# Kernel tuning notes

Measured on AMD Instinct MI355X. Metric: run time of the kernel, lower is better.

## Reference

```python
import jax, jax.numpy as jnp
import numpy as np

B, C, H, W = 4, 256, 48, 48
KD, NH, AR = 32, 8, 4
D = AR * KD            # 128, value dim per head
NHKD = NH * KD         # 256
DH = NH * D            # 1024
EPS = 1e-5


def _bn(y, g, b):
    # BN with fresh running stats (mean=0, var=1): y*g/sqrt(1+eps)+b, over channel dim
    s = g / jnp.sqrt(jnp.float32(1.0) + EPS)
    return y * s[None, :, None] + b[None, :, None]


def setup_inputs() -> dict:
    key = jax.random.key(0)
    ks = jax.random.split(key, 13)
    w = lambda k, sh: jax.random.normal(k, sh, jnp.float32) * 0.05
    g = lambda k, sh: 1.0 + jax.random.normal(k, sh, jnp.float32) * 0.05
    return {
        "x": jax.random.normal(ks[0], (B, C, H, W), jnp.float32),
        "wq": w(ks[1], (NHKD, C)), "gq": g(ks[2], (NHKD,)), "bq": w(ks[3], (NHKD,)),
        "wk": w(ks[4], (NHKD, C)), "gk": g(ks[5], (NHKD,)), "bk": w(ks[6], (NHKD,)),
        "wv": w(ks[7], (DH, C)),   "gv": g(ks[8], (DH,)),   "bv": w(ks[9], (DH,)),
        "wp": w(ks[10], (C, DH)),  "gp": g(ks[11], (C,)),   "bp": w(ks[12], (C,)),
    }


def reference(x, wq, gq, bq, wk, gk, bk, wv, gv, bv, wp, gp, bp):
    b, c, h, w = x.shape
    n = h * w
    xf = x.reshape(b, c, n)                                   # [B,C,N]
    # 1x1 conv == channel matmul, then BN
    q = _bn(jnp.einsum('oc,bcn->bon', wq, xf), gq, bq).reshape(b, NH, KD, n)
    k = _bn(jnp.einsum('oc,bcn->bon', wk, xf), gk, bk).reshape(b, NH, KD, n)
    v = _bn(jnp.einsum('oc,bcn->bon', wv, xf), gv, bv).reshape(b, NH, D, n)
    # NOTE: original forward does NOT apply self.scale
    attn = jax.nn.softmax(jnp.einsum('bhkn,bhkm->bhnm', q, k), axis=-1)  # [B,H,N,N]
    xx = jnp.einsum('bhnm,bhdm->bhdn', attn, v).reshape(b, DH, n)        # [B,DH,N]
    out = _bn(jnp.einsum('oc,bcn->bon', wp, jax.nn.relu(xx)), gp, bp)
    return out.reshape(b, c, h, w)
```

## Files before the change

kernel.cpp:

```cpp
#include <hip/hip_runtime.h>

#define BB 4
#define C 256
#define HW 2304
#define NH 8
#define KD 32
#define D 128
#define DH 1024
#define MQ 256

typedef unsigned short bf16u;
typedef __attribute__((ext_vector_type(8))) short short8;
typedef __attribute__((ext_vector_type(4))) short bfx4;
typedef __attribute__((ext_vector_type(4))) float f32x4;

__device__ __forceinline__ float b2f(bf16u u) {
    return __uint_as_float(((unsigned)u) << 16);
}
__device__ __forceinline__ bf16u f2b(float f) {
    unsigned u = __float_as_uint(f);
    return (bf16u)((u + 0x7fffu + ((u >> 16) & 1u)) >> 16);
}
__device__ __forceinline__ unsigned pk2(float a, float b) {
    return ((unsigned)f2b(b) << 16) | (unsigned)f2b(a);
}

#if __has_builtin(__builtin_amdgcn_mfma_f32_16x16x16bf16_1k)
__device__ __forceinline__ f32x4 mfma16(bfx4 a, bfx4 b, f32x4 c) {
    return __builtin_amdgcn_mfma_f32_16x16x16bf16_1k(a, b, c, 0, 0, 0);
}
#else
__device__ __forceinline__ f32x4 mfma16(bfx4 a, bfx4 b, f32x4 c) {
    asm volatile("v_mfma_f32_16x16x16_bf16 %0, %1, %2, %0"
                 : "+v"(c) : "v"(a), "v"(b));
    return c;
}
#endif

__device__ __forceinline__ void glds16(const bf16u* g, bf16u* l) {
    __builtin_amdgcn_global_load_lds(
        (const __attribute__((address_space(1))) unsigned int*)g,
        (__attribute__((address_space(3))) unsigned int*)l,
        16, 0, 0);
}

__global__ __launch_bounds__(256) void xtrans(const float* __restrict__ x,
                                              bf16u* __restrict__ xT)
{
    const int c0 = blockIdx.x * 64, n0 = blockIdx.y * 64, b = blockIdx.z;
    const int t = threadIdx.x;
    __shared__ float tile[64][68];

    const float* xb = x + (size_t)b * C * HW;
    #pragma unroll
    for (int rr = 0; rr < 4; ++rr) {
        const int cl = rr*16 + (t >> 4);
        float4 v = *(const float4*)(xb + (size_t)(c0 + cl) * HW + n0 + (t & 15)*4);
        tile[cl][(t&15)*4+0] = v.x; tile[cl][(t&15)*4+1] = v.y;
        tile[cl][(t&15)*4+2] = v.z; tile[cl][(t&15)*4+3] = v.w;
    }
    __syncthreads();
    const int nl = t >> 2, ch = t & 3;
    short8 v0, v1;
    #pragma unroll
    for (int kk = 0; kk < 8; ++kk) v0[kk] = (short)f2b(tile[ch*16+kk][nl]);
    #pragma unroll
    for (int kk = 0; kk < 8; ++kk) v1[kk] = (short)f2b(tile[ch*16+8+kk][nl]);
    bf16u* dst = xT + ((size_t)b*HW + n0 + nl) * C + c0 + ch*16;
    *(short8*)(dst)     = v0;
    *(short8*)(dst + 8) = v1;
}

__global__ __launch_bounds__(256, 2) void qkv_gemm(
    const float* __restrict__ wq, const float* __restrict__ wk, const float* __restrict__ wv,
    const float* __restrict__ gq, const float* __restrict__ bq,
    const float* __restrict__ gk, const float* __restrict__ bk,
    const float* __restrict__ gv, const float* __restrict__ bv,
    const bf16u* __restrict__ xT,
    bf16u* __restrict__ qT, bf16u* __restrict__ kT, bf16u* __restrict__ vO)
{
    const int mt = blockIdx.x, ntb = blockIdx.y, b = blockIdx.z;
    const int r0 = mt * 128, c0 = ntb * 128;
    const int t = threadIdx.x, w = t >> 6, l = t & 63;
    const int l15 = l & 15, q = l >> 4;
    const int wr = w >> 1, wc = w & 1;

    const float* wsel; int rloc;
    if (r0 < 256)      { wsel = wq; rloc = r0; }
    else if (r0 < 512) { wsel = wk; rloc = r0 - 256; }
    else               { wsel = wv; rloc = r0 - 512; }

    __shared__ bf16u smem[16384];

    const bf16u* xb = xT + (size_t)b * HW * C;

    const int sA0 = (w*2+0)*64 + l, sA1 = (w*2+1)*64 + l;
    const float* gA0 = wsel + (size_t)(rloc + (sA0>>2)) * C + (sA0&3)*8;
    const float* gA1 = wsel + (size_t)(rloc + (sA1>>2)) * C + (sA1&3)*8;
    const bf16u* gB0 = xb + (size_t)(c0 + (sA0>>2)) * C + (sA0&3)*8;
    const bf16u* gB1 = xb + (size_t)(c0 + (sA1>>2)) * C + (sA1&3)*8;

    f32x4 acc[4][4];
    #pragma unroll
    for (int i = 0; i < 4; ++i)
        #pragma unroll
        for (int j = 0; j < 4; ++j) { acc[i][j][0]=0.f; acc[i][j][1]=0.f; acc[i][j][2]=0.f; acc[i][j][3]=0.f; }

    auto stageB = [&](int k0, int bb) {
        bf16u* Bs = smem + 8192 + bb*4096;
        glds16(gB0 + k0, Bs + (w*2+0)*512);
        glds16(gB1 + k0, Bs + (w*2+1)*512);
    };
    auto stageA = [&](int k0, int bb) {
        bf16u* As = smem + bb*4096;
        #pragma unroll
        for (int jj = 0; jj < 2; ++jj) {
            const float* ga = jj ? gA1 : gA0;
            const int    s  = jj ? sA1 : sA0;
            float4 a = *(const float4*)(ga + k0);
            float4 c = *(const float4*)(ga + k0 + 4);
            short8 v;
            v[0]=(short)f2b(a.x); v[1]=(short)f2b(a.y); v[2]=(short)f2b(a.z); v[3]=(short)f2b(a.w);
            v[4]=(short)f2b(c.x); v[5]=(short)f2b(c.y); v[6]=(short)f2b(c.z); v[7]=(short)f2b(c.w);
            *(short8*)(As + s*8) = v;
        }
    };

    stageB(0, 0); stageA(0, 0);
    for (int it = 0; it < 8; ++it) {
        __syncthreads();
        if (it < 7) { stageB((it+1)*32, (it+1)&1); stageA((it+1)*32, (it+1)&1); }
        const bf16u* A = smem + (it&1)*4096;
        const bf16u* B = smem + 8192 + (it&1)*4096;
        short8 af[4], bf[4];
        #pragma unroll
        for (int i = 0; i < 4; ++i) af[i] = *(const short8*)(A + (wr*64 + i*16 + l15)*32 + q*8);
        #pragma unroll
        for (int j = 0; j < 4; ++j) bf[j] = *(const short8*)(B + (wc*64 + j*16 + l15)*32 + q*8);
        #pragma unroll
        for (int i = 0; i < 4; ++i)
            #pragma unroll
            for (int j = 0; j < 4; ++j)
                acc[i][j] = __builtin_amdgcn_mfma_f32_16x16x32_bf16(af[i], bf[j], acc[i][j], 0, 0, 0);
    }

    const float rs = rsqrtf(1.0f + 1e-5f);
    int ncol[4];
    #pragma unroll
    for (int j = 0; j < 4; ++j) ncol[j] = c0 + wc*64 + j*16 + l15;

    if (r0 < 512) {
        const float* g   = (r0 < 256) ? gq : gk;
        const float* bb_ = (r0 < 256) ? bq : bk;
        bf16u* dst = (r0 < 256) ? qT : kT;
        const int ocb = (r0 & 255) + wr*64;
        #pragma unroll
        for (int i = 0; i < 4; ++i)
            #pragma unroll
            for (int r = 0; r < 4; ++r) {
                const int oc = ocb + i*16 + q*4 + r;
                const float s = g[oc]*rs, bi = bb_[oc];
                const size_t base = ((size_t)(b*NH + (oc>>5)) * HW) * KD + (oc & 31);
                #pragma unroll
                for (int j = 0; j < 4; ++j)
                    dst[base + (size_t)ncol[j]*KD] = f2b(acc[i][j][r]*s + bi);
            }
    } else {
        const int db = (r0 - 512) + wr*64;
        bf16u* dst = vO + (size_t)b * DH * HW;
        #pragma unroll
        for (int i = 0; i < 4; ++i)
            #pragma unroll
            for (int r = 0; r < 4; ++r) {
                const int d = db + i*16 + q*4 + r;
                const float s = gv[d]*rs, bi = bv[d];
                #pragma unroll
                for (int j = 0; j < 4; ++j)
                    dst[(size_t)d*HW + ncol[j]] = f2b(acc[i][j][r]*s + bi);
            }
    }
}

__global__ __launch_bounds__(256, 3) void attn_mfma(
    const bf16u* __restrict__ qT, const bf16u* __restrict__ kT,
    const bf16u* __restrict__ vg, bf16u* __restrict__ xg)
{
    const int nt = blockIdx.x, h = blockIdx.y, b = blockIdx.z;
    const int n0 = nt * 128;
    const int t = threadIdx.x;
    const int w = t >> 6, l = t & 63, l15 = l & 15, q = l >> 4;

    const bf16u* qTh = qT + (size_t)(b*NH + h) * HW * KD;
    const bf16u* kTh = kT + (size_t)(b*NH + h) * HW * KD;
    const bf16u* vh  = vg + ((size_t)b*DH + (size_t)h*D) * HW;

    __shared__ bf16u smem[20480];

    short8 qf0 = *(const short8*)(qTh + (size_t)(n0 + w*32 +      l15) * KD + q*8);
    short8 qf1 = *(const short8*)(qTh + (size_t)(n0 + w*32 + 16 + l15) * KD + q*8);

    f32x4 o[2][8];
    #pragma unroll
    for (int a = 0; a < 2; ++a)
        #pragma unroll
        for (int d = 0; d < 8; ++d) { o[a][d][0]=0.f; o[a][d][1]=0.f; o[a][d][2]=0.f; o[a][d][3]=0.f; }
    float psum0 = 0.f, psum1 = 0.f;
    const f32x4 zero = {0.f, 0.f, 0.f, 0.f};

    auto stage = [&](int m0, int bb) {
        bf16u* Ks = smem + bb*2048;
        bf16u* Vs = smem + 4096 + bb*8192;
        glds16(kTh + (size_t)m0*KD + (w*64 + l)*8, Ks + w*512);
        #pragma unroll
        for (int j = 0; j < 4; ++j) {
            const int s = (w*4 + j)*64 + l;
            const int d = s >> 3, c = s & 7, cg = c ^ (d & 7);
            glds16(vh + (size_t)d*HW + m0 + cg*8, Vs + (w*4 + j)*512);
        }
    };

    stage(0, 0);
    for (int mt = 0; mt < 36; ++mt) {
        __syncthreads();
        if (mt < 35) stage((mt+1)*64, (mt+1)&1);
        const bf16u* Ks = smem + (mt&1)*2048;
        const bf16u* Vs = smem + 4096 + (mt&1)*8192;

        f32x4 st0[4], st1[4];
        #pragma unroll
        for (int kt = 0; kt < 4; ++kt) {
            short8 kf = *(const short8*)(Ks + (kt*16 + l15)*KD + q*8);
            st0[kt] = __builtin_amdgcn_mfma_f32_16x16x32_bf16(kf, qf0, zero, 0, 0, 0);
            st1[kt] = __builtin_amdgcn_mfma_f32_16x16x32_bf16(kf, qf1, zero, 0, 0, 0);
        }

        bfx4 pk0[4], pk1[4];
        #pragma unroll
        for (int kt = 0; kt < 4; ++kt) {
            float p0 = __expf(st0[kt][0]), p1 = __expf(st0[kt][1]);
            float p2 = __expf(st0[kt][2]), p3 = __expf(st0[kt][3]);
            psum0 += (p0 + p1) + (p2 + p3);
            uint2 uu; uu.x = pk2(p0, p1); uu.y = pk2(p2, p3);
            pk0[kt] = __builtin_bit_cast(bfx4, uu);
            float r0_ = __expf(st1[kt][0]), r1 = __expf(st1[kt][1]);
            float r2 = __expf(st1[kt][2]), r3 = __expf(st1[kt][3]);
            psum1 += (r0_ + r1) + (r2 + r3);
            uint2 vv; vv.x = pk2(r0_, r1); vv.y = pk2(r2, r3);
            pk1[kt] = __builtin_bit_cast(bfx4, vv);
        }

        #pragma unroll
        for (int kt = 0; kt < 4; ++kt) {
            #pragma unroll
            for (int dt = 0; dt < 8; ++dt) {
                const int d = dt*16 + l15;
                const int cm = kt*2 + (q >> 1);
                bfx4 vf = *(const bfx4*)(Vs + d*64 + ((cm ^ (d & 7)) * 8) + (q & 1)*4);
                o[0][dt] = mfma16(pk0[kt], vf, o[0][dt]);
                o[1][dt] = mfma16(pk1[kt], vf, o[1][dt]);
            }
        }
    }

    psum0 += __shfl_xor(psum0, 16); psum0 += __shfl_xor(psum0, 32);
    psum1 += __shfl_xor(psum1, 16); psum1 += __shfl_xor(psum1, 32);
    float inv0[4], inv1[4];
    #pragma unroll
    for (int r = 0; r < 4; ++r) {
        inv0[r] = 1.0f / __shfl(psum0, q*4 + r);
        inv1[r] = 1.0f / __shfl(psum1, q*4 + r);
    }
    __syncthreads();
    bf16u* Od = smem + w * 4352;
    #pragma unroll
    for (int dt = 0; dt < 8; ++dt)
        #pragma unroll
        for (int r = 0; r < 4; ++r) {
            float v0 = fmaxf(o[0][dt][r] * inv0[r], 0.f);
            float v1 = fmaxf(o[1][dt][r] * inv1[r], 0.f);
            Od[(     q*4 + r)*136 + dt*16 + l15] = f2b(v0);
            Od[(16 + q*4 + r)*136 + dt*16 + l15] = f2b(v1);
        }
    bf16u* xb = xg + ((size_t)b*HW + n0 + w*32) * DH + h*D;
    #pragma unroll
    for (int rr = 0; rr < 2; ++rr) {
        const int row = rr*16 + (l >> 2), c = l & 3;
        #pragma unroll
        for (int kk = 0; kk < 4; ++kk)
            *(short8*)(xb + (size_t)row*DH + c*32 + kk*8) =
                *(const short8*)(Od + row*136 + c*32 + kk*8);
    }
}

__global__ __launch_bounds__(256, 4) void out_gemm(
    const float* __restrict__ wp, const float* __restrict__ gp, const float* __restrict__ bp,
    const bf16u* __restrict__ xx, float* __restrict__ out)
{
    const int mt = blockIdx.x, ntb = blockIdx.y, b = blockIdx.z;
    const int r0 = mt * 64, c0 = ntb * 64;
    const int t = threadIdx.x, w = t >> 6, l = t & 63;
    const int l15 = l & 15, q = l >> 4;
    const int wr = w >> 1, wc = w & 1;

    __shared__ bf16u smem[8192];

    const bf16u* xb = xx + (size_t)b * HW * DH;

    const float* gA = wp + (size_t)(r0 + (t>>2)) * DH + (t&3)*8;
    const bf16u* gB = xb + (size_t)(c0 + (t>>2)) * DH + (t&3)*8;

    f32x4 acc[2][2];
    #pragma unroll
    for (int i = 0; i < 2; ++i)
        #pragma unroll
        for (int j = 0; j < 2; ++j) { acc[i][j][0]=0.f; acc[i][j][1]=0.f; acc[i][j][2]=0.f; acc[i][j][3]=0.f; }

    auto stage = [&](int k0, int bb) {
        glds16(gB + k0, smem + 4096 + bb*2048 + w*512);
        float4 a = *(const float4*)(gA + k0);
        float4 c = *(const float4*)(gA + k0 + 4);
        short8 v;
        v[0]=(short)f2b(a.x); v[1]=(short)f2b(a.y); v[2]=(short)f2b(a.z); v[3]=(short)f2b(a.w);
        v[4]=(short)f2b(c.x); v[5]=(short)f2b(c.y); v[6]=(short)f2b(c.z); v[7]=(short)f2b(c.w);
        *(short8*)(smem + bb*2048 + t*8) = v;
    };

    stage(0, 0);
    for (int it = 0; it < 32; ++it) {
        __syncthreads();
        if (it < 31) stage((it+1)*32, (it+1)&1);
        const bf16u* A = smem + (it&1)*2048;
        const bf16u* B = smem + 4096 + (it&1)*2048;
        short8 af[2], bf[2];
        #pragma unroll
        for (int i = 0; i < 2; ++i) af[i] = *(const short8*)(A + (wr*32 + i*16 + l15)*32 + q*8);
        #pragma unroll
        for (int j = 0; j < 2; ++j) bf[j] = *(const short8*)(B + (wc*32 + j*16 + l15)*32 + q*8);
        #pragma unroll
        for (int i = 0; i < 2; ++i)
            #pragma unroll
            for (int j = 0; j < 2; ++j)
                acc[i][j] = __builtin_amdgcn_mfma_f32_16x16x32_bf16(af[i], bf[j], acc[i][j], 0, 0, 0);
    }

    const float rs = rsqrtf(1.0f + 1e-5f);
    #pragma unroll
    for (int i = 0; i < 2; ++i)
        #pragma unroll
        for (int r = 0; r < 4; ++r) {
            const int oc = r0 + wr*32 + i*16 + q*4 + r;
            const float s = gp[oc]*rs, bi = bp[oc];
            #pragma unroll
            for (int j = 0; j < 2; ++j) {
                const int n = c0 + wc*32 + j*16 + l15;
                out[((size_t)b*C + oc)*HW + n] = acc[i][j][r]*s + bi;
            }
        }
}

extern "C" void kernel_launch(void* const* d_in, const int* in_sizes, int n_in,
                              void* d_out, int out_size, void* d_ws, size_t ws_size,
                              hipStream_t stream) {
    const float* x  = (const float*)d_in[0];
    const float* wq = (const float*)d_in[1];
    const float* gq = (const float*)d_in[2];
    const float* bq = (const float*)d_in[3];
    const float* wk = (const float*)d_in[4];
    const float* gk = (const float*)d_in[5];
    const float* bk = (const float*)d_in[6];
    const float* wv = (const float*)d_in[7];
    const float* gv = (const float*)d_in[8];
    const float* bv = (const float*)d_in[9];
    const float* wp = (const float*)d_in[10];
    const float* gp = (const float*)d_in[11];
    const float* bp = (const float*)d_in[12];
    float* out = (float*)d_out;

    bf16u* qw = (bf16u*)d_ws;
    bf16u* kw = qw + (size_t)BB * MQ * HW;
    bf16u* vw = kw + (size_t)BB * MQ * HW;
    bf16u* xw = vw + (size_t)BB * DH * HW;
    bf16u* xTb = xw;

    hipLaunchKernelGGL(xtrans, dim3(4, 36, BB), dim3(256), 0, stream, x, xTb);
    hipLaunchKernelGGL(qkv_gemm, dim3(12, 18, BB), dim3(256), 0, stream,
                       wq, wk, wv, gq, bq, gk, bk, gv, bv, xTb, qw, kw, vw);
    hipLaunchKernelGGL(attn_mfma, dim3(18, NH, BB), dim3(256), 0, stream,
                       qw, kw, vw, xw);
    hipLaunchKernelGGL(out_gemm, dim3(4, 36, BB), dim3(256), 0, stream,
                       wp, gp, bp, xw, out);
}
```

Measured before the change: 239.4 us.

## Pre-fold BN into bf16 weights, triple-buffer GEMMs, coalesce QKV stores, use exp2

A new prep kernel converts the Q/K/V weights to bf16 once per call. It folds the BN scale into them, plus a log2(e) factor for Q, and writes a combined bias vector. This lets qkv_gemm stage both operands with direct global-to-LDS loads in a three-stage pipeline. The QKV epilogue now goes through LDS with a swizzled layout so Q/K/V are written as 16-byte coalesced stores instead of scattered 2-byte writes. Attention switches to exp2 and 16x16x32 MFMAs for the PV product, and out_gemm uses 64-wide K tiles with triple buffering; this costs an extra launch and more LDS per block.

```diff
diff --git a/kernel.cpp b/kernel.cpp
--- a/kernel.cpp
+++ b/kernel.cpp
@@ -13,35 +13,64 @@
 typedef __attribute__((ext_vector_type(8))) short short8;
 typedef __attribute__((ext_vector_type(4))) short bfx4;
 typedef __attribute__((ext_vector_type(4))) float f32x4;
-
-__device__ __forceinline__ float b2f(bf16u u) {
-    return __uint_as_float(((unsigned)u) << 16);
-}
+typedef __attribute__((ext_vector_type(4))) unsigned ux4;
+typedef __attribute__((ext_vector_type(2))) unsigned ux2;
+
+union U8 { ux4 u; short8 s; };
+union V8 { short8 s; bfx4 h[2]; };
+
 __device__ __forceinline__ bf16u f2b(float f) {
     unsigned u = __float_as_uint(f);
     return (bf16u)((u + 0x7fffu + ((u >> 16) & 1u)) >> 16);
 }
-__device__ __forceinline__ unsigned pk2(float a, float b) {
-    return ((unsigned)f2b(b) << 16) | (unsigned)f2b(a);
-}
-
-#if __has_builtin(__builtin_amdgcn_mfma_f32_16x16x16bf16_1k)
-__device__ __forceinline__ f32x4 mfma16(bfx4 a, bfx4 b, f32x4 c) {
-    return __builtin_amdgcn_mfma_f32_16x16x16bf16_1k(a, b, c, 0, 0, 0);
-}
-#else
-__device__ __forceinline__ f32x4 mfma16(bfx4 a, bfx4 b, f32x4 c) {
-    asm volatile("v_mfma_f32_16x16x16_bf16 %0, %1, %2, %0"
-                 : "+v"(c) : "v"(a), "v"(b));
-    return c;
-}
-#endif
+__device__ __forceinline__ unsigned pkb(float a, float b) {
+    return __builtin_amdgcn_perm(__float_as_uint(b) + 0x8000u,
+                                 __float_as_uint(a) + 0x8000u, 0x07060302u);
+}
 
 __device__ __forceinline__ void glds16(const bf16u* g, bf16u* l) {
     __builtin_amdgcn_global_load_lds(
         (const __attribute__((address_space(1))) unsigned int*)g,
         (__attribute__((address_space(3))) unsigned int*)l,
         16, 0, 0);
+}
+
+#define MFMA32 __builtin_amdgcn_mfma_f32_16x16x32_bf16
+
+__global__ __launch_bounds__(256) void prep(
+    const float* __restrict__ wq, const float* __restrict__ wk, const float* __restrict__ wv,
+    const float* __restrict__ gq, const float* __restrict__ bq,
+    const float* __restrict__ gk, const float* __restrict__ bk,
+    const float* __restrict__ gv, const float* __restrict__ bv,
+    bf16u* __restrict__ Wc, float* __restrict__ biasc)
+{
+    const float rs = rsqrtf(1.0f + 1e-5f);
+    const float L2E = 1.4426950408889634f;
+    const int t = threadIdx.x, blk = blockIdx.x;
+    if (blk < 192) {
+        const int idx = (blk*256 + t) * 8;
+        const int row = idx >> 8;
+        const float* src; float sc;
+        if (idx < 65536)       { src = wq + idx;            sc = gq[row]*rs*L2E; }
+        else if (idx < 131072) { src = wk + (idx - 65536);  sc = gk[row-256]*rs; }
+        else                   { src = wv + (idx - 131072); sc = gv[row-512]*rs; }
+        float4 a = *(const float4*)(src);
+        float4 c = *(const float4*)(src + 4);
+        ux4 v;
+        v.x = pkb(a.x*sc, a.y*sc); v.y = pkb(a.z*sc, a.w*sc);
+        v.z = pkb(c.x*sc, c.y*sc); v.w = pkb(c.z*sc, c.w*sc);
+        *(ux4*)(Wc + idx) = v;
+    } else {
+        #pragma unroll
+        for (int k = 0; k < 6; ++k) {
+            const int r = k*256 + t;
+            float v;
+            if (r < 256)      v = bq[r] * L2E;
+            else if (r < 512) v = bk[r - 256];
+            else              v = bv[r - 512];
+            biasc[r] = v;
+        }
+    }
 }
 
 __global__ __launch_bounds__(256) void xtrans(const float* __restrict__ x,
@@ -71,11 +100,8 @@
     *(short8*)(dst + 8) = v1;
 }
 
-__global__ __launch_bounds__(256, 2) void qkv_gemm(
-    const float* __restrict__ wq, const float* __restrict__ wk, const float* __restrict__ wv,
-    const float* __restrict__ gq, const float* __restrict__ bq,
-    const float* __restrict__ gk, const float* __restrict__ bk,
-    const float* __restrict__ gv, const float* __restrict__ bv,
+__global__ __launch_bounds__(256, 3) void qkv_gemm(
+    const bf16u* __restrict__ Wc, const float* __restrict__ biasc,
     const bf16u* __restrict__ xT,
     bf16u* __restrict__ qT, bf16u* __restrict__ kT, bf16u* __restrict__ vO)
 {
@@ -85,18 +111,13 @@
     const int l15 = l & 15, q = l >> 4;
     const int wr = w >> 1, wc = w & 1;
 
-    const float* wsel; int rloc;
-    if (r0 < 256)      { wsel = wq; rloc = r0; }
-    else if (r0 < 512) { wsel = wk; rloc = r0 - 256; }
-    else               { wsel = wv; rloc = r0 - 512; }
-
-    __shared__ bf16u smem[16384];
+    __shared__ bf16u smem[24576];
 
     const bf16u* xb = xT + (size_t)b * HW * C;
 
     const int sA0 = (w*2+0)*64 + l, sA1 = (w*2+1)*64 + l;
-    const float* gA0 = wsel + (size_t)(rloc + (sA0>>2)) * C + (sA0&3)*8;
-    const float* gA1 = wsel + (size_t)(rloc + (sA1>>2)) * C + (sA1&3)*8;
+    const bf16u* gA0 = Wc + (size_t)(r0 + (sA0>>2)) * C + (sA0&3)*8;
+    const bf16u* gA1 = Wc + (size_t)(r0 + (sA1>>2)) * C + (sA1&3)*8;
     const bf16u* gB0 = xb + (size_t)(c0 + (sA0>>2)) * C + (sA0&3)*8;
     const bf16u* gB1 = xb + (size_t)(c0 + (sA1>>2)) * C + (sA1&3)*8;
 
@@ -106,78 +127,101 @@
         #pragma unroll
         for (int j = 0; j < 4; ++j) { acc[i][j][0]=0.f; acc[i][j][1]=0.f; acc[i][j][2]=0.f; acc[i][j][3]=0.f; }
 
-    auto stageB = [&](int k0, int bb) {
-        bf16u* Bs = smem + 8192 + bb*4096;
+    auto stage = [&](int it2, int bb) {
+        const int k0 = it2 * 32;
+        bf16u* As = smem + bb*4096;
+        bf16u* Bs = smem + 12288 + bb*4096;
+        glds16(gA0 + k0, As + (w*2+0)*512);
+        glds16(gA1 + k0, As + (w*2+1)*512);
         glds16(gB0 + k0, Bs + (w*2+0)*512);
         glds16(gB1 + k0, Bs + (w*2+1)*512);
     };
-    auto stageA = [&](int k0, int bb) {
-        bf16u* As = smem + bb*4096;
-        #pragma unroll
-        for (int jj = 0; jj < 2; ++jj) {
-            const float* ga = jj ? gA1 : gA0;
-            const int    s  = jj ? sA1 : sA0;
-            float4 a = *(const float4*)(ga + k0);
-            float4 c = *(const float4*)(ga + k0 + 4);
-            short8 v;
-            v[0]=(short)f2b(a.x); v[1]=(short)f2b(a.y); v[2]=(short)f2b(a.z); v[3]=(short)f2b(a.w);
-            v[4]=(short)f2b(c.x); v[5]=(short)f2b(c.y); v[6]=(short)f2b(c.z); v[7]=(short)f2b(c.w);
-            *(short8*)(As + s*8) = v;
-        }
-    };
-
-    stageB(0, 0); stageA(0, 0);
+
+    const bool isV = (r0 >= 512);
+    stage(0, 0); stage(1, 1);
     for (int it = 0; it < 8; ++it) {
         __syncthreads();
-        if (it < 7) { stageB((it+1)*32, (it+1)&1); stageA((it+1)*32, (it+1)&1); }
-        const bf16u* A = smem + (it&1)*4096;
-        const bf16u* B = smem + 8192 + (it&1)*4096;
+        if (it + 2 < 8) stage(it + 2, (it + 2) % 3);
+        const bf16u* A = smem + (it % 3) * 4096;
+        const bf16u* B = smem + 12288 + (it % 3) * 4096;
         short8 af[4], bf[4];
         #pragma unroll
         for (int i = 0; i < 4; ++i) af[i] = *(const short8*)(A + (wr*64 + i*16 + l15)*32 + q*8);
         #pragma unroll
         for (int j = 0; j < 4; ++j) bf[j] = *(const short8*)(B + (wc*64 + j*16 + l15)*32 + q*8);
-        #pragma unroll
-        for (int i = 0; i < 4; ++i)
-            #pragma unroll
-            for (int j = 0; j < 4; ++j)
-                acc[i][j] = __builtin_amdgcn_mfma_f32_16x16x32_bf16(af[i], bf[j], acc[i][j], 0, 0, 0);
-    }
-
-    const float rs = rsqrtf(1.0f + 1e-5f);
-    int ncol[4];
-    #pragma unroll
-    for (int j = 0; j < 4; ++j) ncol[j] = c0 + wc*64 + j*16 + l15;
-
-    if (r0 < 512) {
-        const float* g   = (r0 < 256) ? gq : gk;
-        const float* bb_ = (r0 < 256) ? bq : bk;
-        bf16u* dst = (r0 < 256) ? qT : kT;
-        const int ocb = (r0 & 255) + wr*64;
-        #pragma unroll
-        for (int i = 0; i < 4; ++i)
-            #pragma unroll
-            for (int r = 0; r < 4; ++r) {
-                const int oc = ocb + i*16 + q*4 + r;
-                const float s = g[oc]*rs, bi = bb_[oc];
-                const size_t base = ((size_t)(b*NH + (oc>>5)) * HW) * KD + (oc & 31);
+        if (!isV) {
+            #pragma unroll
+            for (int i = 0; i < 4; ++i)
                 #pragma unroll
                 for (int j = 0; j < 4; ++j)
-                    dst[base + (size_t)ncol[j]*KD] = f2b(acc[i][j][r]*s + bi);
-            }
-    } else {
-        const int db = (r0 - 512) + wr*64;
-        bf16u* dst = vO + (size_t)b * DH * HW;
-        #pragma unroll
-        for (int i = 0; i < 4; ++i)
-            #pragma unroll
-            for (int r = 0; r < 4; ++r) {
-                const int d = db + i*16 + q*4 + r;
-                const float s = gv[d]*rs, bi = bv[d];
+                    acc[i][j] = MFMA32(af[i], bf[j], acc[i][j], 0, 0, 0);
+        } else {
+            #pragma unroll
+            for (int i = 0; i < 4; ++i)
                 #pragma unroll
                 for (int j = 0; j < 4; ++j)
-                    dst[(size_t)d*HW + ncol[j]] = f2b(acc[i][j][r]*s + bi);
+                    acc[i][j] = MFMA32(bf[j], af[i], acc[i][j], 0, 0, 0);
+        }
+    }
+
+    __syncthreads();
+    bf16u* Od = smem + w * 4096;
+
+    if (!isV) {
+        float bC[4][4];
+        #pragma unroll
+        for (int i = 0; i < 4; ++i)
+            #pragma unroll
+            for (int r = 0; r < 4; ++r)
+                bC[i][r] = biasc[r0 + wr*64 + i*16 + q*4 + r];
+        #pragma unroll
+        for (int i = 0; i < 4; ++i)
+            #pragma unroll
+            for (int j = 0; j < 4; ++j) {
+                float y0 = acc[i][j][0] + bC[i][0];
+                float y1 = acc[i][j][1] + bC[i][1];
+                float y2 = acc[i][j][2] + bC[i][2];
+                float y3 = acc[i][j][3] + bC[i][3];
+                ux2 pk; pk.x = pkb(y0, y1); pk.y = pkb(y2, y3);
+                const int row = j*16 + l15;
+                const int ch  = (i*2 + (q >> 1)) ^ (l15 & 7);
+                *(ux2*)(Od + row*64 + ch*8 + (q & 1)*4) = pk;
             }
+        bf16u* dst = (r0 < 256) ? qT : kT;
+        const int n = c0 + wc*64 + l;
+        #pragma unroll
+        for (int c = 0; c < 8; ++c) {
+            short8 v = *(const short8*)(Od + l*64 + ((c ^ (l & 7)) * 8));
+            const int ocg = (r0 & 255) + wr*64 + c*8;
+            const int h = ocg >> 5, kd0 = ocg & 31;
+            *(short8*)(dst + ((size_t)(b*NH + h) * HW + n) * KD + kd0) = v;
+        }
+    } else {
+        float bC[4];
+        #pragma unroll
+        for (int i = 0; i < 4; ++i)
+            bC[i] = biasc[r0 + wr*64 + i*16 + l15];
+        #pragma unroll
+        for (int i = 0; i < 4; ++i)
+            #pragma unroll
+            for (int j = 0; j < 4; ++j) {
+                float y0 = acc[i][j][0] + bC[i];
+                float y1 = acc[i][j][1] + bC[i];
+                float y2 = acc[i][j][2] + bC[i];
+                float y3 = acc[i][j][3] + bC[i];
+                ux2 pk; pk.x = pkb(y0, y1); pk.y = pkb(y2, y3);
+                const int row = i*16 + l15;
+                const int ch  = (j*2 + (q >> 1)) ^ (l15 & 7);
+                *(ux2*)(Od + row*64 + ch*8 + (q & 1)*4) = pk;
+            }
+        bf16u* dst = vO + (size_t)b * DH * HW;
+        const int d = (r0 - 512) + wr*64 + l;
+        #pragma unroll
+        for (int c = 0; c < 8; ++c) {
+            short8 v = *(const short8*)(Od + l*64 + ((c ^ (l & 7)) * 8));
+            const int n = c0 + wc*64 + c*8;
+            *(short8*)(dst + (size_t)d * HW + n) = v;
+        }
     }
 }
 
@@ -230,34 +274,45 @@
         #pragma unroll
         for (int kt = 0; kt < 4; ++kt) {
             short8 kf = *(const short8*)(Ks + (kt*16 + l15)*KD + q*8);
-            st0[kt] = __builtin_amdgcn_mfma_f32_16x16x32_bf16(kf, qf0, zero, 0, 0, 0);
-            st1[kt] = __builtin_amdgcn_mfma_f32_16x16x32_bf16(kf, qf1, zero, 0, 0, 0);
-        }
-
-        bfx4 pk0[4], pk1[4];
+            st0[kt] = MFMA32(kf, qf0, zero, 0, 0, 0);
+            st1[kt] = MFMA32(kf, qf1, zero, 0, 0, 0);
+        }
+
+        unsigned dA0[4], dB0[4], dA1[4], dB1[4];
         #pragma unroll
         for (int kt = 0; kt < 4; ++kt) {
-            float p0 = __expf(st0[kt][0]), p1 = __expf(st0[kt][1]);
-            float p2 = __expf(st0[kt][2]), p3 = __expf(st0[kt][3]);
+            float p0 = __builtin_amdgcn_exp2f(st0[kt][0]);
+            float p1 = __builtin_amdgcn_exp2f(st0[kt][1]);
+            float p2 = __builtin_amdgcn_exp2f(st0[kt][2]);
+            float p3 = __builtin_amdgcn_exp2f(st0[kt][3]);
             psum0 += (p0 + p1) + (p2 + p3);
-            uint2 uu; uu.x = pk2(p0, p1); uu.y = pk2(p2, p3);
-            pk0[kt] = __builtin_bit_cast(bfx4, uu);
-            float r0_ = __expf(st1[kt][0]), r1 = __expf(st1[kt][1]);
-            float r2 = __expf(st1[kt][2]), r3 = __expf(st1[kt][3]);
-            psum1 += (r0_ + r1) + (r2 + r3);
-            uint2 vv; vv.x = pk2(r0_, r1); vv.y = pk2(r2, r3);
-            pk1[kt] = __builtin_bit_cast(bfx4, vv);
-        }
-
-        #pragma unroll
-        for (int kt = 0; kt < 4; ++kt) {
+            dA0[kt] = pkb(p0, p1); dB0[kt] = pkb(p2, p3);
+            float r0_ = __builtin_amdgcn_exp2f(st1[kt][0]);
+            float r1_ = __builtin_amdgcn_exp2f(st1[kt][1]);
+            float r2_ = __builtin_amdgcn_exp2f(st1[kt][2]);
+            float r3_ = __builtin_amdgcn_exp2f(st1[kt][3]);
+            psum1 += (r0_ + r1_) + (r2_ + r3_);
+            dA1[kt] = pkb(r0_, r1_); dB1[kt] = pkb(r2_, r3_);
+        }
+
+        #pragma unroll
+        for (int kh = 0; kh < 2; ++kh) {
+            U8 u0, u1;
+            u0.u[0] = dA0[kh*2];   u0.u[1] = dB0[kh*2];
+            u0.u[2] = dA0[kh*2+1]; u0.u[3] = dB0[kh*2+1];
+            u1.u[0] = dA1[kh*2];   u1.u[1] = dB1[kh*2];
+            u1.u[2] = dA1[kh*2+1]; u1.u[3] = dB1[kh*2+1];
+            const int clo = kh*4 + (q >> 1);
+            const int chi = clo + 2;
+            const int sub = (q & 1) * 4;
             #pragma unroll
             for (int dt = 0; dt < 8; ++dt) {
                 const int d = dt*16 + l15;
-                const int cm = kt*2 + (q >> 1);
-                bfx4 vf = *(const bfx4*)(Vs + d*64 + ((cm ^ (d & 7)) * 8) + (q & 1)*4);
-                o[0][dt] = mfma16(pk0[kt], vf, o[0][dt]);
-                o[1][dt] = mfma16(pk1[kt], vf, o[1][dt]);
+                V8 vv;
+                vv.h[0] = *(const bfx4*)(Vs + d*64 + ((clo ^ (d & 7)) * 8) + sub);
+                vv.h[1] = *(const bfx4*)(Vs + d*64 + ((chi ^ (d & 7)) * 8) + sub);
+                o[0][dt] = MFMA32(u0.s, vv.s, o[0][dt], 0, 0, 0);
+                o[1][dt] = MFMA32(u1.s, vv.s, o[1][dt], 0, 0, 0);
             }
         }
     }
@@ -292,7 +347,7 @@
     }
 }
 
-__global__ __launch_bounds__(256, 4) void out_gemm(
+__global__ __launch_bounds__(256, 3) void out_gemm(
     const float* __restrict__ wp, const float* __restrict__ gp, const float* __restrict__ bp,
     const bf16u* __restrict__ xx, float* __restrict__ out)
 {
@@ -302,12 +357,16 @@
     const int l15 = l & 15, q = l >> 4;
     const int wr = w >> 1, wc = w & 1;
 
-    __shared__ bf16u smem[8192];
+    __shared__ bf16u smem[24576];
 
     const bf16u* xb = xx + (size_t)b * HW * DH;
 
-    const float* gA = wp + (size_t)(r0 + (t>>2)) * DH + (t&3)*8;
-    const bf16u* gB = xb + (size_t)(c0 + (t>>2)) * DH + (t&3)*8;
+    const int sA0 = t, sA1 = 256 + t;
+    const float* gA0 = wp + (size_t)(r0 + (sA0>>3)) * DH + (sA0&7)*8;
+    const float* gA1 = wp + (size_t)(r0 + (sA1>>3)) * DH + (sA1&7)*8;
+    const int sB0 = w*128 + l, sB1 = w*128 + 64 + l;
+    const bf16u* gB0 = xb + (size_t)(c0 + (sB0>>3)) * DH + (sB0&7)*8;
+    const bf16u* gB1 = xb + (size_t)(c0 + (sB1>>3)) * DH + (sB1&7)*8;
 
     f32x4 acc[2][2];
     #pragma unroll
@@ -315,32 +374,44 @@
         #pragma unroll
         for (int j = 0; j < 2; ++j) { acc[i][j][0]=0.f; acc[i][j][1]=0.f; acc[i][j][2]=0.f; acc[i][j][3]=0.f; }
 
-    auto stage = [&](int k0, int bb) {
-        glds16(gB + k0, smem + 4096 + bb*2048 + w*512);
-        float4 a = *(const float4*)(gA + k0);
-        float4 c = *(const float4*)(gA + k0 + 4);
-        short8 v;
-        v[0]=(short)f2b(a.x); v[1]=(short)f2b(a.y); v[2]=(short)f2b(a.z); v[3]=(short)f2b(a.w);
-        v[4]=(short)f2b(c.x); v[5]=(short)f2b(c.y); v[6]=(short)f2b(c.z); v[7]=(short)f2b(c.w);
-        *(short8*)(smem + bb*2048 + t*8) = v;
+    auto stage = [&](int it2, int bb) {
+        const int k0 = it2 * 64;
+        bf16u* As = smem + bb*4096;
+        bf16u* Bs = smem + 12288 + bb*4096;
+        glds16(gB0 + k0, Bs + (w*2+0)*512);
+        glds16(gB1 + k0, Bs + (w*2+1)*512);
+        #pragma unroll
+        for (int jj = 0; jj < 2; ++jj) {
+            const float* ga = jj ? gA1 : gA0;
+            const int    s  = jj ? sA1 : sA0;
+            float4 a = *(const float4*)(ga + k0);
+            float4 c = *(const float4*)(ga + k0 + 4);
+            ux4 v;
+            v.x = pkb(a.x, a.y); v.y = pkb(a.z, a.w);
+            v.z = pkb(c.x, c.y); v.w = pkb(c.z, c.w);
+            *(ux4*)(As + s*8) = v;
+        }
     };
 
-    stage(0, 0);
-    for (int it = 0; it < 32; ++it) {
+    stage(0, 0); stage(1, 1);
+    for (int it = 0; it < 16; ++it) {
         __syncthreads();
-        if (it < 31) stage((it+1)*32, (it+1)&1);
-        const bf16u* A = smem + (it&1)*2048;
-        const bf16u* B = smem + 4096 + (it&1)*2048;
-        short8 af[2], bf[2];
-        #pragma unroll
-        for (int i = 0; i < 2; ++i) af[i] = *(const short8*)(A + (wr*32 + i*16 + l15)*32 + q*8);
-        #pragma unroll
-        for (int j = 0; j < 2; ++j) bf[j] = *(const short8*)(B + (wc*32 + j*16 + l15)*32 + q*8);
-        #pragma unroll
-        for (int i = 0; i < 2; ++i)
-            #pragma unroll
-            for (int j = 0; j < 2; ++j)
-                acc[i][j] = __builtin_amdgcn_mfma_f32_16x16x32_bf16(af[i], bf[j], acc[i][j], 0, 0, 0);
+        if (it + 2 < 16) stage(it + 2, (it + 2) % 3);
+        const bf16u* A = smem + (it % 3) * 4096;
+        const bf16u* B = smem + 12288 + (it % 3) * 4096;
+        #pragma unroll
+        for (int kk = 0; kk < 2; ++kk) {
+            short8 af[2], bf[2];
+            #pragma unroll
+            for (int i = 0; i < 2; ++i) af[i] = *(const short8*)(A + (wr*32 + i*16 + l15)*64 + kk*32 + q*8);
+            #pragma unroll
+            for (int j = 0; j < 2; ++j) bf[j] = *(const short8*)(B + (wc*32 + j*16 + l15)*64 + kk*32 + q*8);
+            #pragma unroll
+            for (int i = 0; i < 2; ++i)
+                #pragma unroll
+                for (int j = 0; j < 2; ++j)
+                    acc[i][j] = MFMA32(af[i], bf[j], acc[i][j], 0, 0, 0);
+        }
     }
 
     const float rs = rsqrtf(1.0f + 1e-5f);
@@ -381,10 +452,14 @@
     bf16u* vw = kw + (size_t)BB * MQ * HW;
     bf16u* xw = vw + (size_t)BB * DH * HW;
     bf16u* xTb = xw;
-
+    bf16u* Wc  = xw + (size_t)BB * MQ * HW;
+    float* biasc = (float*)(Wc + 393216);
+
+    hipLaunchKernelGGL(prep, dim3(193), dim3(256), 0, stream,
+                       wq, wk, wv, gq, bq, gk, bk, gv, bv, Wc, biasc);
     hipLaunchKernelGGL(xtrans, dim3(4, 36, BB), dim3(256), 0, stream, x, xTb);
     hipLaunchKernelGGL(qkv_gemm, dim3(12, 18, BB), dim3(256), 0, stream,
-                       wq, wk, wv, gq, bq, gk, bk, gv, bv, xTb, qw, kw, vw);
+                       Wc, biasc, xTb, qw, kw, vw);
     hipLaunchKernelGGL(attn_mfma, dim3(18, NH, BB), dim3(256), 0, stream,
                        qw, kw, vw, xw);
     hipLaunchKernelGGL(out_gemm, dim3(4, 36, BB), dim3(256), 0, stream,
```

Result: faster. 213.7 us (-10.8%).
